# Kernel optimization log

Measured on AMD Instinct MI355X. Metric: run time of the kernel, lower is better.

## Reference

```python
import jax, jax.numpy as jnp
import numpy as np

B, TAU, T0V, D, PD, RD, DO, K = 2048, 32, 96, 64, 3, 1, 64, 16
R = 1.0  # radius for radius_graph


def setup_inputs() -> dict:
    key = jax.random.key(0)
    ks = jax.random.split(key, 9)
    return {
        "x": jax.random.normal(ks[0], (B, TAU, D), jnp.float32),
        "pos": jax.random.uniform(ks[1], (B, TAU, PD), jnp.float32),
        "rot": jax.random.uniform(ks[2], (B, TAU, RD), jnp.float32),
        "old_x": jax.random.normal(ks[3], (B, 128, D), jnp.float32),
        "old_pos": jax.random.uniform(ks[4], (B, 128, PD), jnp.float32),
        "old_rot": jax.random.uniform(ks[5], (B, 128, RD), jnp.float32),
        "W_self": jax.random.normal(ks[6], (D + PD + RD, DO), jnp.float32) * 0.1,
        "W_nbr": jax.random.normal(ks[7], (D + PD + RD, DO), jnp.float32) * 0.1,
        "bias": jax.random.normal(ks[8], (DO,), jnp.float32) * 0.1,
        "T0": T0V,
        "tau": TAU,
    }


def reference(x, pos, rot, old_x, old_pos, old_rot, W_self, W_nbr, bias, T0, tau):
    # --- update(): scatter new observations into the state buffers ---
    # (regular case: T[b]=T0, taus[b]=tau for all b, so new_idx is a static slice)
    new_x = old_x.at[:, T0:T0 + tau].set(x)
    new_pos = old_pos.at[:, T0:T0 + tau].set(pos)
    new_rot = old_rot.at[:, T0:T0 + tau].set(rot)

    L = T0 + tau  # valid (non-padded) nodes per env
    nx, npv, nr = new_x[:, :L], new_pos[:, :L], new_rot[:, :L]
    h = jnp.concatenate([nx, npv, nr], axis=-1)  # [B, L, D+PD+RD] node features

    # --- radius_graph(r, max_num_neighbors=K, loop=True) + remove_noncausal_edges ---
    # edge (j -> i) kept iff ||pos_j - pos_i|| <= r and j < i (causal, drops self-loops)
    diff = npv[:, :, None, :] - npv[:, None, :, :]           # [B, L, L, PD]
    d2 = jnp.sum(diff * diff, axis=-1)                        # [B, L, L] (target i, source j)
    t_idx = jnp.arange(L)
    causal = t_idx[None, :] < t_idx[:, None]                  # [L, L] j < i
    mask = causal[None, :, :] & (d2 <= R * R)
    masked_d2 = jnp.where(mask, d2, jnp.inf)
    neg_d, nbr_idx = jax.lax.top_k(-masked_d2, K)             # k nearest causal in-radius
    valid = jnp.isfinite(neg_d)                               # [B, L, K]

    # --- gnn(): one message-passing layer (stand-in for external gnn) ---
    msg = h @ W_nbr                                           # [B, L, DO]
    gathered = jax.vmap(lambda m, i: m[i])(msg, nbr_idx)      # [B, L, K, DO]
    agg = jnp.sum(gathered * valid[..., None].astype(msg.dtype), axis=2)
    out = jax.nn.relu(h @ W_self + agg + bias)                # [B, L, DO]

    # --- gather flat_new_idx / scatter into padded output ---
    padded_output = out[:, T0:T0 + tau]                       # [B, tau, DO]
    return padded_output, new_x, new_pos, new_rot
```

## Files before the change

kernel.cpp:

```cpp
#include <hip/hip_runtime.h>
#include <hip/hip_bf16.h>
#include <cstdint>
#include <cstddef>

#define NB 2048
#define TAU 32
#define T0C 96
#define LQ 128
#define DD 64
#define DOUT 64
#define KK 16
#define INVK 0xFFFFFFFFu

typedef unsigned long long u64;
typedef unsigned int u32;
typedef __attribute__((ext_vector_type(8))) short short8;
typedef __attribute__((ext_vector_type(4))) float f32x4;

__device__ __forceinline__ float fmul_exact(float a, float b) {
  float r; asm("v_mul_f32 %0, %1, %2" : "=v"(r) : "v"(a), "v"(b)); return r;
}
__device__ __forceinline__ float fadd_exact(float a, float b) {
  float r; asm("v_add_f32 %0, %1, %2" : "=v"(r) : "v"(a), "v"(b)); return r;
}
__device__ __forceinline__ unsigned short f2bf(float f) {
  __hip_bfloat16 h = __float2bfloat16(f);
  return *reinterpret_cast<unsigned short*>(&h);
}
__device__ __forceinline__ u32 shfl_xor_u32(u32 v, int mask) {
  return (u32)__shfl_xor((int)v, mask, 64);
}

__device__ __forceinline__ void barrier_lgkm() {
  asm volatile("s_waitcnt lgkmcnt(0)" ::: "memory");
  __builtin_amdgcn_s_barrier();
  __builtin_amdgcn_sched_barrier(0);
}

#define CA(i, j) { u32 _lo = min(kd[i], kd[j]); u32 _hi = max(kd[i], kd[j]); kd[i] = _lo; kd[j] = _hi; }
#define CD(i, j) { u32 _lo = min(kd[i], kd[j]); u32 _hi = max(kd[i], kd[j]); kd[i] = _hi; kd[j] = _lo; }

#define SORT16() do { \
  CA(0,1)  CD(2,3)  CA(4,5)  CD(6,7)  CA(8,9)  CD(10,11) CA(12,13) CD(14,15) \
  CA(0,2)  CA(1,3)  CD(4,6)  CD(5,7)  CA(8,10) CA(9,11)  CD(12,14) CD(13,15) \
  CA(0,1)  CA(2,3)  CD(4,5)  CD(6,7)  CA(8,9)  CA(10,11) CD(12,13) CD(14,15) \
  CA(0,4)  CA(1,5)  CA(2,6)  CA(3,7)  CD(8,12) CD(9,13)  CD(10,14) CD(11,15) \
  CA(0,2)  CA(1,3)  CA(4,6)  CA(5,7)  CD(8,10) CD(9,11)  CD(12,14) CD(13,15) \
  CA(0,1)  CA(2,3)  CA(4,5)  CA(6,7)  CD(8,9)  CD(10,11) CD(12,13) CD(14,15) \
  CA(0,8)  CA(1,9)  CA(2,10) CA(3,11) CA(4,12) CA(5,13)  CA(6,14)  CA(7,15)  \
  CA(0,4)  CA(1,5)  CA(2,6)  CA(3,7)  CA(8,12) CA(9,13)  CA(10,14) CA(11,15) \
  CA(0,2)  CA(1,3)  CA(4,6)  CA(5,7)  CA(8,10) CA(9,11)  CA(12,14) CA(13,15) \
  CA(0,1)  CA(2,3)  CA(4,5)  CA(6,7)  CA(8,9)  CA(10,11) CA(12,13) CA(14,15) \
} while (0)

#define MERGE16() do { \
  CA(0,8)  CA(1,9)  CA(2,10) CA(3,11) CA(4,12) CA(5,13)  CA(6,14)  CA(7,15)  \
  CA(0,4)  CA(1,5)  CA(2,6)  CA(3,7)  CA(8,12) CA(9,13)  CA(10,14) CA(11,15) \
  CA(0,2)  CA(1,3)  CA(4,6)  CA(5,7)  CA(8,10) CA(9,11)  CA(12,14) CA(13,15) \
  CA(0,1)  CA(2,3)  CA(4,5)  CA(6,7)  CA(8,9)  CA(10,11) CA(12,13) CA(14,15) \
} while (0)

#define SHUF_MERGE(mask) do { \
  u32 pb[16]; \
  _Pragma("unroll") \
  for (int _i = 0; _i < 16; ++_i) pb[_i] = shfl_xor_u32(kd[15 - _i], mask); \
  _Pragma("unroll") \
  for (int _i = 0; _i < 16; ++_i) kd[_i] = min(kd[_i], pb[_i]); \
  MERGE16(); \
} while (0)

__global__ __launch_bounds__(256) void prep_w(
    const float* __restrict__ W_nbr, const float* __restrict__ W_self,
    unsigned short* __restrict__ wst) {
  int idx = blockIdx.x * 256 + threadIdx.x;
  int m = idx & 4095;
  int n = m >> 6, k = m & 63;
  const float* src = (idx < 4096) ? W_nbr : W_self;
  wst[idx] = f2bf(src[k * DOUT + n]);
}

__global__ __launch_bounds__(256, 4) void navgcm_fused(
    const float* __restrict__ x, const float* __restrict__ pos_in, const float* __restrict__ rot_in,
    const float* __restrict__ old_x, const float* __restrict__ old_pos, const float* __restrict__ old_rot,
    const float* __restrict__ W_self, const float* __restrict__ W_nbr, const float* __restrict__ bias,
    const unsigned short* __restrict__ wst,
    float* __restrict__ outp)
{
  const int b = blockIdx.x;
  const int tid = threadIdx.x;
  const int lane = tid & 63;
  const int wv = tid >> 6;
  const int fr = lane & 15;
  const int fg = lane >> 4;

  __shared__ __align__(16) unsigned char uni[18432];
  __shared__ __align__(16) unsigned short Pm[32][136];
  __shared__ float px[LQ], py[LQ], pz[LQ], rt[LQ];

  unsigned short (*Hs)[72] = reinterpret_cast<unsigned short(*)[72]>(uni);
  unsigned short (*msgsT)[136] = reinterpret_cast<unsigned short(*)[136]>(uni);

  const bool haspos = tid < LQ;
  float p0 = 0.f, p1 = 0.f, p2 = 0.f, rr = 0.f;
  if (haspos) {
    int t = tid;
    if (t < T0C) {
      const float* s = old_pos + ((size_t)b * LQ + t) * 3;
      p0 = s[0]; p1 = s[1]; p2 = s[2];
      rr = old_rot[(size_t)b * LQ + t];
    } else {
      const float* s = pos_in + ((size_t)b * TAU + (t - T0C)) * 3;
      p0 = s[0]; p1 = s[1]; p2 = s[2];
      rr = rot_in[(size_t)b * TAU + (t - T0C)];
    }
  }

  float4 v[8];
  #pragma unroll
  for (int it = 0; it < 8; ++it) {
    int n = tid + 256 * it;
    int row = n >> 4, c4 = n & 15;
    const float4* src = (row < T0C)
        ? (const float4*)(old_x + ((size_t)b * LQ + row) * DD)
        : (const float4*)(x + ((size_t)b * TAU + (row - T0C)) * DD);
    v[it] = src[c4];
  }

  {
    u32* pz32 = (u32*)&Pm[0][0];
    #pragma unroll
    for (int k = 0; k < 9; ++k) {
      int idx = tid + 256 * k;
      if (idx < 2176) pz32[idx] = 0u;
    }
  }

  float* dpos = outp + (size_t)NB * TAU * DOUT + (size_t)NB * LQ * DD;
  float* drot = dpos + (size_t)NB * LQ * 3;
  if (haspos) {
    px[tid] = p0; py[tid] = p1; pz[tid] = p2; rt[tid] = rr;
    size_t g = (size_t)b * LQ + tid;
    dpos[g * 3 + 0] = p0; dpos[g * 3 + 1] = p1; dpos[g * 3 + 2] = p2;
    drot[g] = rr;
  }
  barrier_lgkm();

  {
    const int q = tid >> 3, s8 = tid & 7;
    const int i = T0C + q;
    const float pix = px[i], piy = py[i], piz = pz[i];

    u32 kb[16];
    #pragma unroll
    for (int c = 0; c < 16; ++c) {
      int j = 8 * c + s8;
      float dx = pix - px[j], dy = piy - py[j], dz = piz - pz[j];
      float d2 = fadd_exact(fadd_exact(fmul_exact(dx, dx), fmul_exact(dy, dy)),
                            fmul_exact(dz, dz));
      bool valid = (d2 <= 1.0f) && (j < i);
      kb[c] = valid ? __float_as_uint(d2) : INVK;
    }

    u32 kd[16];
    #pragma unroll
    for (int c = 0; c < 16; ++c) kd[c] = kb[c];
    SORT16();
    SHUF_MERGE(1);
    SHUF_MERGE(2);
    SHUF_MERGE(4);

    const u32 T = kd[15];
    int nless = 0;
    #pragma unroll
    for (int t = 0; t < KK; ++t) nless += (kd[t] < T) ? 1 : 0;
    const int needT = (T == INVK) ? 0 : (KK - nless);

    u32 selmask = 0;
    #pragma unroll
    for (int c = 0; c < 16; ++c) selmask |= (kb[c] < T) ? (1u << c) : 0u;

    u32 em = 0;
    #pragma unroll
    for (int c = 0; c < 16; ++c) em |= (kb[c] == T) ? (1u << c) : 0u;
    if (T == INVK) em = 0;
    for (int t = 0; __any(t < needT); ++t) {
      bool act = t < needT;
      u32 myj = (act && em) ? (u32)(8 * __builtin_ctz(em) + s8) : 0xFFFFu;
      u32 gj = myj;
      gj = min(gj, shfl_xor_u32(gj, 1));
      gj = min(gj, shfl_xor_u32(gj, 2));
      gj = min(gj, shfl_xor_u32(gj, 4));
      if (act && myj == gj && myj != 0xFFFFu) {
        int c = __builtin_ctz(em);
        selmask |= 1u << c;
        em &= em - 1;
      }
    }

    u32 m = selmask;
    while (m) {
      int c = __builtin_ctz(m);
      m &= m - 1;
      Pm[q][8 * c + s8] = 0x3F80;
    }
  }

  float4* dnx = (float4*)(outp + (size_t)NB * TAU * DOUT);
  #pragma unroll
  for (int it = 0; it < 8; ++it) {
    int n = tid + 256 * it;
    int row = n >> 4, c4 = n & 15;
    ushort4 w4;
    w4.x = f2bf(v[it].x); w4.y = f2bf(v[it].y); w4.z = f2bf(v[it].z); w4.w = f2bf(v[it].w);
    *reinterpret_cast<ushort4*>(&Hs[row][c4 * 4]) = w4;
    dnx[(size_t)b * 2048 + n] = v[it];
  }
  barrier_lgkm();

  const unsigned short* wn_t = wst;
  const unsigned short* ws_t = wst + 4096;

  short8 bW[4][2];
  #pragma unroll
  for (int nt = 0; nt < 4; ++nt)
    #pragma unroll
    for (int ks = 0; ks < 2; ++ks)
      bW[nt][ks] = *reinterpret_cast<const short8*>(&wn_t[(nt * 16 + fr) * 64 + ks * 32 + fg * 8]);

  f32x4 acc[2][4];
  #pragma unroll
  for (int m = 0; m < 2; ++m)
    #pragma unroll
    for (int n = 0; n < 4; ++n)
      acc[m][n] = (f32x4){0.f, 0.f, 0.f, 0.f};

  #pragma unroll
  for (int mtl = 0; mtl < 2; ++mtl) {
    int mrow = (2 * wv + mtl) * 16;
    short8 a0 = *reinterpret_cast<const short8*>(&Hs[mrow + fr][fg * 8]);
    short8 a1 = *reinterpret_cast<const short8*>(&Hs[mrow + fr][32 + fg * 8]);
    #pragma unroll
    for (int nt = 0; nt < 4; ++nt) {
      acc[mtl][nt] = __builtin_amdgcn_mfma_f32_16x16x32_bf16(a0, bW[nt][0], acc[mtl][nt], 0, 0, 0);
      acc[mtl][nt] = __builtin_amdgcn_mfma_f32_16x16x32_bf16(a1, bW[nt][1], acc[mtl][nt], 0, 0, 0);
    }
  }

  const int mt = wv & 1;
  const int ntb = (wv >> 1) * 2;
  short8 aQ0 = *reinterpret_cast<const short8*>(&Hs[T0C + mt * 16 + fr][fg * 8]);
  short8 aQ1 = *reinterpret_cast<const short8*>(&Hs[T0C + mt * 16 + fr][32 + fg * 8]);
  f32x4 acc2[2];
  #pragma unroll
  for (int n = 0; n < 2; ++n) acc2[n] = (f32x4){0.f, 0.f, 0.f, 0.f};
  #pragma unroll
  for (int ntl = 0; ntl < 2; ++ntl) {
    int nt = ntb + ntl;
    short8 b0 = *reinterpret_cast<const short8*>(&ws_t[(nt * 16 + fr) * 64 + fg * 8]);
    short8 b1 = *reinterpret_cast<const short8*>(&ws_t[(nt * 16 + fr) * 64 + 32 + fg * 8]);
    acc2[ntl] = __builtin_amdgcn_mfma_f32_16x16x32_bf16(aQ0, b0, acc2[ntl], 0, 0, 0);
    acc2[ntl] = __builtin_amdgcn_mfma_f32_16x16x32_bf16(aQ1, b1, acc2[ntl], 0, 0, 0);
  }
  barrier_lgkm();

  float wn4[4][4];
  #pragma unroll
  for (int nt = 0; nt < 4; ++nt) {
    int col = nt * 16 + fr;
    wn4[nt][0] = W_nbr[64 * DOUT + col];
    wn4[nt][1] = W_nbr[65 * DOUT + col];
    wn4[nt][2] = W_nbr[66 * DOUT + col];
    wn4[nt][3] = W_nbr[67 * DOUT + col];
  }
  #pragma unroll
  for (int mtl = 0; mtl < 2; ++mtl) {
    int rowb = (2 * wv + mtl) * 16 + fg * 4;
    float q0[4], q1[4], q2[4], q3[4];
    #pragma unroll
    for (int r = 0; r < 4; ++r) {
      q0[r] = px[rowb + r]; q1[r] = py[rowb + r];
      q2[r] = pz[rowb + r]; q3[r] = rt[rowb + r];
    }
    #pragma unroll
    for (int nt = 0; nt < 4; ++nt) {
      int col = nt * 16 + fr;
      ushort4 w4;
      unsigned short* wp = (unsigned short*)&w4;
      #pragma unroll
      for (int r = 0; r < 4; ++r) {
        float vv = acc[mtl][nt][r]
                 + q0[r] * wn4[nt][0] + q1[r] * wn4[nt][1]
                 + q2[r] * wn4[nt][2] + q3[r] * wn4[nt][3];
        wp[r] = f2bf(vv);
      }
      if (rowb + 3 == LQ - 1) wp[3] = 0;
      *reinterpret_cast<ushort4*>(&msgsT[col][rowb]) = w4;
    }
  }
  barrier_lgkm();

  f32x4 agg4[2];
  #pragma unroll
  for (int n = 0; n < 2; ++n) agg4[n] = (f32x4){0.f, 0.f, 0.f, 0.f};
  #pragma unroll
  for (int ks = 0; ks < 4; ++ks) {
    short8 pa = *reinterpret_cast<const short8*>(&Pm[mt * 16 + fr][ks * 32 + fg * 8]);
    #pragma unroll
    for (int ntl = 0; ntl < 2; ++ntl) {
      int col16 = (ntb + ntl) * 16 + fr;
      short8 pb = *reinterpret_cast<const short8*>(&msgsT[col16][ks * 32 + fg * 8]);
      agg4[ntl] = __builtin_amdgcn_mfma_f32_16x16x32_bf16(pa, pb, agg4[ntl], 0, 0, 0);
    }
  }

  #pragma unroll
  for (int ntl = 0; ntl < 2; ++ntl) {
    int col = (ntb + ntl) * 16 + fr;
    float ws0 = W_self[64 * DOUT + col], ws1 = W_self[65 * DOUT + col];
    float ws2 = W_self[66 * DOUT + col], ws3 = W_self[67 * DOUT + col];
    float bi = bias[col];
    #pragma unroll
    for (int r = 0; r < 4; ++r) {
      int q = mt * 16 + fg * 4 + r;
      int row = T0C + q;
      float vv = acc2[ntl][r] + agg4[ntl][r] + bi
               + px[row] * ws0 + py[row] * ws1 + pz[row] * ws2 + rt[row] * ws3;
      vv = fmaxf(vv, 0.f);
      outp[((size_t)b * TAU + q) * DOUT + col] = vv;
    }
  }
}

extern "C" void kernel_launch(void* const* d_in, const int* in_sizes, int n_in,
                              void* d_out, int out_size, void* d_ws, size_t ws_size,
                              hipStream_t stream) {
  (void)in_sizes; (void)n_in; (void)ws_size; (void)out_size;
  const float* x       = (const float*)d_in[0];
  const float* pos     = (const float*)d_in[1];
  const float* rot     = (const float*)d_in[2];
  const float* old_x   = (const float*)d_in[3];
  const float* old_pos = (const float*)d_in[4];
  const float* old_rot = (const float*)d_in[5];
  const float* W_self  = (const float*)d_in[6];
  const float* W_nbr   = (const float*)d_in[7];
  const float* bias    = (const float*)d_in[8];
  float* out = (float*)d_out;
  unsigned short* wst = (unsigned short*)d_ws;

  hipLaunchKernelGGL(prep_w, dim3(32), dim3(256), 0, stream, W_nbr, W_self, wst);
  hipLaunchKernelGGL(navgcm_fused, dim3(NB), dim3(256), 0, stream,
                     x, pos, rot, old_x, old_pos, old_rot, W_self, W_nbr, bias, wst, out);
}
```

Baseline: 40.65 us.

## Reassociate neighbor aggregation: sum neighbor features first, then multiply by W_nbr

Instead of computing messages for all 128 nodes (H·W_nbr) and then aggregating with the adjacency matrix, the kernel first aggregates raw node features (P·H) for the 32 query rows and then multiplies the 32x64 result by W_nbr. Position and rotation contributions are aggregated separately per query via shuffles. H is stored transposed with an XOR swizzle to serve as the B operand. This removes the 128-row message GEMM and one barrier, at the cost of an extra bf16 rounding of aggregated features and different numerics.

```diff
diff --git a/kernel.cpp b/kernel.cpp
--- a/kernel.cpp
+++ b/kernel.cpp
@@ -12,7 +12,6 @@
 #define KK 16
 #define INVK 0xFFFFFFFFu
 
-typedef unsigned long long u64;
 typedef unsigned int u32;
 typedef __attribute__((ext_vector_type(8))) short short8;
 typedef __attribute__((ext_vector_type(4))) float f32x4;
@@ -93,12 +92,12 @@
   const int fr = lane & 15;
   const int fg = lane >> 4;
 
-  __shared__ __align__(16) unsigned char uni[18432];
+  __shared__ __align__(16) unsigned short HsT[64 * 136];
+  __shared__ __align__(16) unsigned short Hq[32 * 72];
+  __shared__ __align__(16) unsigned short Gl[32 * 72];
   __shared__ __align__(16) unsigned short Pm[32][136];
   __shared__ float px[LQ], py[LQ], pz[LQ], rt[LQ];
-
-  unsigned short (*Hs)[72] = reinterpret_cast<unsigned short(*)[72]>(uni);
-  unsigned short (*msgsT)[136] = reinterpret_cast<unsigned short(*)[136]>(uni);
+  __shared__ float4 Gpos[32];
 
   const bool haspos = tid < LQ;
   float p0 = 0.f, p1 = 0.f, p2 = 0.f, rr = 0.f;
@@ -203,6 +202,23 @@
       m &= m - 1;
       Pm[q][8 * c + s8] = 0x3F80;
     }
+
+    float g0 = 0.f, g1 = 0.f, g2 = 0.f, g3 = 0.f;
+    u32 m2 = selmask;
+    while (m2) {
+      int c = __builtin_ctz(m2);
+      m2 &= m2 - 1;
+      int j = 8 * c + s8;
+      g0 += px[j]; g1 += py[j]; g2 += pz[j]; g3 += rt[j];
+    }
+    g0 += __shfl_xor(g0, 1, 64); g0 += __shfl_xor(g0, 2, 64); g0 += __shfl_xor(g0, 4, 64);
+    g1 += __shfl_xor(g1, 1, 64); g1 += __shfl_xor(g1, 2, 64); g1 += __shfl_xor(g1, 4, 64);
+    g2 += __shfl_xor(g2, 1, 64); g2 += __shfl_xor(g2, 2, 64); g2 += __shfl_xor(g2, 4, 64);
+    g3 += __shfl_xor(g3, 1, 64); g3 += __shfl_xor(g3, 2, 64); g3 += __shfl_xor(g3, 4, 64);
+    if (s8 == 0) {
+      float4 gv; gv.x = g0; gv.y = g1; gv.z = g2; gv.w = g3;
+      Gpos[q] = gv;
+    }
   }
 
   float4* dnx = (float4*)(outp + (size_t)NB * TAU * DOUT);
@@ -210,46 +226,43 @@
   for (int it = 0; it < 8; ++it) {
     int n = tid + 256 * it;
     int row = n >> 4, c4 = n & 15;
-    ushort4 w4;
-    w4.x = f2bf(v[it].x); w4.y = f2bf(v[it].y); w4.z = f2bf(v[it].z); w4.w = f2bf(v[it].w);
-    *reinterpret_cast<ushort4*>(&Hs[row][c4 * 4]) = w4;
+    unsigned short w0 = f2bf(v[it].x), w1 = f2bf(v[it].y),
+                   w2 = f2bf(v[it].z), w3 = f2bf(v[it].w);
+    int rj = row ^ ((c4 & 7) << 3);
+    HsT[(4 * c4 + 0) * 136 + rj] = w0;
+    HsT[(4 * c4 + 1) * 136 + rj] = w1;
+    HsT[(4 * c4 + 2) * 136 + rj] = w2;
+    HsT[(4 * c4 + 3) * 136 + rj] = w3;
+    if (it >= 6) {
+      ushort4 w4; w4.x = w0; w4.y = w1; w4.z = w2; w4.w = w3;
+      *reinterpret_cast<ushort4*>(&Hq[(row - T0C) * 72 + c4 * 4]) = w4;
+    }
     dnx[(size_t)b * 2048 + n] = v[it];
   }
   barrier_lgkm();
 
   const unsigned short* wn_t = wst;
   const unsigned short* ws_t = wst + 4096;
-
-  short8 bW[4][2];
-  #pragma unroll
-  for (int nt = 0; nt < 4; ++nt)
-    #pragma unroll
-    for (int ks = 0; ks < 2; ++ks)
-      bW[nt][ks] = *reinterpret_cast<const short8*>(&wn_t[(nt * 16 + fr) * 64 + ks * 32 + fg * 8]);
-
-  f32x4 acc[2][4];
-  #pragma unroll
-  for (int m = 0; m < 2; ++m)
-    #pragma unroll
-    for (int n = 0; n < 4; ++n)
-      acc[m][n] = (f32x4){0.f, 0.f, 0.f, 0.f};
-
-  #pragma unroll
-  for (int mtl = 0; mtl < 2; ++mtl) {
-    int mrow = (2 * wv + mtl) * 16;
-    short8 a0 = *reinterpret_cast<const short8*>(&Hs[mrow + fr][fg * 8]);
-    short8 a1 = *reinterpret_cast<const short8*>(&Hs[mrow + fr][32 + fg * 8]);
-    #pragma unroll
-    for (int nt = 0; nt < 4; ++nt) {
-      acc[mtl][nt] = __builtin_amdgcn_mfma_f32_16x16x32_bf16(a0, bW[nt][0], acc[mtl][nt], 0, 0, 0);
-      acc[mtl][nt] = __builtin_amdgcn_mfma_f32_16x16x32_bf16(a1, bW[nt][1], acc[mtl][nt], 0, 0, 0);
-    }
-  }
-
   const int mt = wv & 1;
   const int ntb = (wv >> 1) * 2;
-  short8 aQ0 = *reinterpret_cast<const short8*>(&Hs[T0C + mt * 16 + fr][fg * 8]);
-  short8 aQ1 = *reinterpret_cast<const short8*>(&Hs[T0C + mt * 16 + fr][32 + fg * 8]);
+
+  f32x4 accG[2];
+  #pragma unroll
+  for (int n = 0; n < 2; ++n) accG[n] = (f32x4){0.f, 0.f, 0.f, 0.f};
+  #pragma unroll
+  for (int ks = 0; ks < 4; ++ks) {
+    short8 pa = *reinterpret_cast<const short8*>(&Pm[mt * 16 + fr][ks * 32 + fg * 8]);
+    #pragma unroll
+    for (int ntl = 0; ntl < 2; ++ntl) {
+      int nf = (ntb + ntl) * 16 + fr;
+      int j0 = (ks * 32 + fg * 8) ^ (((nf >> 2) & 7) << 3);
+      short8 hb = *reinterpret_cast<const short8*>(&HsT[nf * 136 + j0]);
+      accG[ntl] = __builtin_amdgcn_mfma_f32_16x16x32_bf16(pa, hb, accG[ntl], 0, 0, 0);
+    }
+  }
+
+  short8 aQ0 = *reinterpret_cast<const short8*>(&Hq[(mt * 16 + fr) * 72 + fg * 8]);
+  short8 aQ1 = *reinterpret_cast<const short8*>(&Hq[(mt * 16 + fr) * 72 + 32 + fg * 8]);
   f32x4 acc2[2];
   #pragma unroll
   for (int n = 0; n < 2; ++n) acc2[n] = (f32x4){0.f, 0.f, 0.f, 0.f};
@@ -261,61 +274,40 @@
     acc2[ntl] = __builtin_amdgcn_mfma_f32_16x16x32_bf16(aQ0, b0, acc2[ntl], 0, 0, 0);
     acc2[ntl] = __builtin_amdgcn_mfma_f32_16x16x32_bf16(aQ1, b1, acc2[ntl], 0, 0, 0);
   }
+
+  #pragma unroll
+  for (int ntl = 0; ntl < 2; ++ntl) {
+    int nf = (ntb + ntl) * 16 + fr;
+    #pragma unroll
+    for (int r = 0; r < 4; ++r) {
+      int q = mt * 16 + fg * 4 + r;
+      Gl[q * 72 + nf] = f2bf(accG[ntl][r]);
+    }
+  }
   barrier_lgkm();
 
-  float wn4[4][4];
-  #pragma unroll
-  for (int nt = 0; nt < 4; ++nt) {
-    int col = nt * 16 + fr;
-    wn4[nt][0] = W_nbr[64 * DOUT + col];
-    wn4[nt][1] = W_nbr[65 * DOUT + col];
-    wn4[nt][2] = W_nbr[66 * DOUT + col];
-    wn4[nt][3] = W_nbr[67 * DOUT + col];
-  }
-  #pragma unroll
-  for (int mtl = 0; mtl < 2; ++mtl) {
-    int rowb = (2 * wv + mtl) * 16 + fg * 4;
-    float q0[4], q1[4], q2[4], q3[4];
-    #pragma unroll
-    for (int r = 0; r < 4; ++r) {
-      q0[r] = px[rowb + r]; q1[r] = py[rowb + r];
-      q2[r] = pz[rowb + r]; q3[r] = rt[rowb + r];
-    }
-    #pragma unroll
-    for (int nt = 0; nt < 4; ++nt) {
-      int col = nt * 16 + fr;
-      ushort4 w4;
-      unsigned short* wp = (unsigned short*)&w4;
-      #pragma unroll
-      for (int r = 0; r < 4; ++r) {
-        float vv = acc[mtl][nt][r]
-                 + q0[r] * wn4[nt][0] + q1[r] * wn4[nt][1]
-                 + q2[r] * wn4[nt][2] + q3[r] * wn4[nt][3];
-        wp[r] = f2bf(vv);
-      }
-      if (rowb + 3 == LQ - 1) wp[3] = 0;
-      *reinterpret_cast<ushort4*>(&msgsT[col][rowb]) = w4;
-    }
-  }
-  barrier_lgkm();
-
   f32x4 agg4[2];
   #pragma unroll
   for (int n = 0; n < 2; ++n) agg4[n] = (f32x4){0.f, 0.f, 0.f, 0.f};
   #pragma unroll
-  for (int ks = 0; ks < 4; ++ks) {
-    short8 pa = *reinterpret_cast<const short8*>(&Pm[mt * 16 + fr][ks * 32 + fg * 8]);
+  for (int ks = 0; ks < 2; ++ks) {
+    short8 ga = *reinterpret_cast<const short8*>(&Gl[(mt * 16 + fr) * 72 + ks * 32 + fg * 8]);
     #pragma unroll
     for (int ntl = 0; ntl < 2; ++ntl) {
-      int col16 = (ntb + ntl) * 16 + fr;
-      short8 pb = *reinterpret_cast<const short8*>(&msgsT[col16][ks * 32 + fg * 8]);
-      agg4[ntl] = __builtin_amdgcn_mfma_f32_16x16x32_bf16(pa, pb, agg4[ntl], 0, 0, 0);
-    }
-  }
+      short8 wb = *reinterpret_cast<const short8*>(&wn_t[((ntb + ntl) * 16 + fr) * 64 + ks * 32 + fg * 8]);
+      agg4[ntl] = __builtin_amdgcn_mfma_f32_16x16x32_bf16(ga, wb, agg4[ntl], 0, 0, 0);
+    }
+  }
+
+  float4 gpv[4];
+  #pragma unroll
+  for (int r = 0; r < 4; ++r) gpv[r] = Gpos[mt * 16 + fg * 4 + r];
 
   #pragma unroll
   for (int ntl = 0; ntl < 2; ++ntl) {
     int col = (ntb + ntl) * 16 + fr;
+    float wn0 = W_nbr[64 * DOUT + col], wn1 = W_nbr[65 * DOUT + col];
+    float wn2 = W_nbr[66 * DOUT + col], wn3 = W_nbr[67 * DOUT + col];
     float ws0 = W_self[64 * DOUT + col], ws1 = W_self[65 * DOUT + col];
     float ws2 = W_self[66 * DOUT + col], ws3 = W_self[67 * DOUT + col];
     float bi = bias[col];
@@ -324,6 +316,7 @@
       int q = mt * 16 + fg * 4 + r;
       int row = T0C + q;
       float vv = acc2[ntl][r] + agg4[ntl][r] + bi
+               + gpv[r].x * wn0 + gpv[r].y * wn1 + gpv[r].z * wn2 + gpv[r].w * wn3
                + px[row] * ws0 + py[row] * ws1 + pz[row] * ws2 + rt[row] * ws3;
       vv = fmaxf(vv, 0.f);
       outp[((size_t)b * TAU + q) * DOUT + col] = vv;
```

After: 39.02 us. 4.0% less time.
